# Performance work log

Hardware: AMD Instinct MI355X
Metric: run time of the kernel (lower is better)

Reference implementation:

```python
import jax, jax.numpy as jnp
import numpy as np

B, TE, TD, H, D = 8, 2048, 256, 128, 128


def setup_inputs() -> dict:
    key = jax.random.key(0)
    k1, k2, k3, k4, k5 = jax.random.split(key, 5)
    he = lambda k, shape: jax.random.normal(k, shape, dtype=jnp.float32) * jnp.sqrt(2.0 / shape[0])
    return {
        "encoder_out_seq": jax.random.normal(k1, (B, TE, H), dtype=jnp.float32),
        "decoder_out_seq": jax.random.normal(k2, (B, TD, D), dtype=jnp.float32),
        "W_a": he(k3, (H, H)),
        "U_a": he(k4, (D, H)),
        "V_a": he(k5, (H, 1)),
    }


def reference(encoder_out_seq, decoder_out_seq, W_a, U_a, V_a):
    # Precompute encoder and decoder projections once (the TF code redundantly
    # recomputes enc@W_a every decoder step inside backend.rnn).
    Wenc = jnp.einsum('bth,hk->btk', encoder_out_seq, W_a)      # [B,Te,H]
    Udec = jnp.einsum('bjd,dk->bjk', decoder_out_seq, U_a)     # [B,Td,H]
    # Additive (Bahdanau) scores: v^T tanh(W s_i + U h_j)
    scores = jnp.einsum('bjtk,k->bjt',
                        jnp.tanh(Wenc[:, None, :, :] + Udec[:, :, None, :]),
                        V_a[:, 0])                              # [B,Td,Te]
    e_outputs = jax.nn.softmax(scores, axis=-1)                 # [B,Td,Te]
    c_outputs = jnp.einsum('bjt,bth->bjh', e_outputs, encoder_out_seq)  # [B,Td,H]
    return c_outputs, e_outputs
```

## Files before the change

kernel.cpp:

```cpp
#include <hip/hip_runtime.h>
#include <stdint.h>

#define B  8
#define TE 2048
#define TD 256
#define H  128

#define FMA4(acc, s, wv) \
  acc.x += (s)*(wv).x; acc.y += (s)*(wv).y; acc.z += (s)*(wv).z; acc.w += (s)*(wv).w

__global__ __launch_bounds__(256) void proj_kernel(
    const float* __restrict__ enc, const float* __restrict__ dec,
    const float* __restrict__ Wa,  const float* __restrict__ Ua,
    float* __restrict__ EgT, float* __restrict__ Fg) {
  __shared__ float Ls[16 * 132];
  const float C2 = 2.8853900817779268f;
  int tid = threadIdx.x;
  int bid = blockIdx.x;
  bool isE = (bid < 1024);
  int rbase = (isE ? bid : bid - 1024) * 16;
  const float* in = isE ? enc : dec;
  const float* Mg = isE ? Wa : Ua;
  int hq = tid & 31, rq = tid >> 5;
  int h0 = hq * 4, r0 = rq * 2;
  const float* rowp = in + (size_t)(rbase + r0) * H;
  const float* wp = Mg + h0;
  float4 a0{0,0,0,0}, a1{0,0,0,0};
  #pragma unroll 2
  for (int kb = 0; kb < 32; ++kb) {
    float4 rv0 = *(const float4*)(rowp + kb * 4);
    float4 rv1 = *(const float4*)(rowp + H + kb * 4);
    float4 w0 = *(const float4*)(wp + (size_t)(4 * kb + 0) * H);
    float4 w1 = *(const float4*)(wp + (size_t)(4 * kb + 1) * H);
    float4 w2 = *(const float4*)(wp + (size_t)(4 * kb + 2) * H);
    float4 w3 = *(const float4*)(wp + (size_t)(4 * kb + 3) * H);
    FMA4(a0, rv0.x, w0); FMA4(a0, rv0.y, w1); FMA4(a0, rv0.z, w2); FMA4(a0, rv0.w, w3);
    FMA4(a1, rv1.x, w0); FMA4(a1, rv1.y, w1); FMA4(a1, rv1.z, w2); FMA4(a1, rv1.w, w3);
  }
  float4 e0, e1;
  e0.x = __builtin_amdgcn_exp2f(a0.x * C2); e0.y = __builtin_amdgcn_exp2f(a0.y * C2);
  e0.z = __builtin_amdgcn_exp2f(a0.z * C2); e0.w = __builtin_amdgcn_exp2f(a0.w * C2);
  e1.x = __builtin_amdgcn_exp2f(a1.x * C2); e1.y = __builtin_amdgcn_exp2f(a1.y * C2);
  e1.z = __builtin_amdgcn_exp2f(a1.z * C2); e1.w = __builtin_amdgcn_exp2f(a1.w * C2);
  if (isE) {
    *(float4*)&Ls[(r0 + 0) * 132 + h0] = e0;
    *(float4*)&Ls[(r0 + 1) * 132 + h0] = e1;
    __syncthreads();
    int b_e = rbase >> 11, t_in = rbase & 2047;
    int tb = t_in >> 6, toff = t_in & 63;
    float* dst = EgT + ((size_t)(b_e * 32 + tb) * 128) * 64 + toff;
    #pragma unroll
    for (int jj = 0; jj < 8; ++jj) {
      int idx = jj * 256 + tid;
      int r = idx & 15, k = idx >> 4;
      dst[(size_t)k * 64 + r] = Ls[r * 132 + k];
    }
  } else {
    int b_f = rbase >> 8, j_in = rbase & 255;
    float* dst = Fg + ((size_t)(b_f * TD + j_in + r0)) * H + h0;
    *(float4*)(dst + 0 * H) = e0;
    *(float4*)(dst + 1 * H) = e1;
  }
}

__global__ __launch_bounds__(512, 4) void fused_kernel(
    const float* __restrict__ EgT, const float* __restrict__ Fg,
    const float* __restrict__ Va,  const float* __restrict__ enc,
    float* __restrict__ oute, float* __restrict__ outc) {
  __shared__ float S[4 * 2048];
  __shared__ float red[16];
  int tid = threadIdx.x;
  int bid = blockIdx.x;
  int b = bid & 7, jt = bid >> 3;
  int j0 = jt * 4;
  int lane = tid & 63, w = tid >> 6;
  const float4* vp = (const float4*)Va;
  float V1 = 0.f;
  #pragma unroll
  for (int q = 0; q < 32; ++q) { float4 v = vp[q]; V1 += v.x + v.y + v.z + v.w; }

  const float4* Fp = (const float4*)(Fg + (size_t)(b * TD + j0) * H);
  const float* Ep[4];
  #pragma unroll
  for (int it = 0; it < 4; ++it)
    Ep[it] = EgT + ((size_t)(b * 32 + w + 8 * it) * 128) * 64 + lane;
  float s[4][4];
  #pragma unroll
  for (int it = 0; it < 4; ++it)
    #pragma unroll
    for (int j = 0; j < 4; ++j) s[it][j] = 0.f;
  float eka[8], ekb[8];

#define LOADE(dst, base, off)                                        \
  { const float* _p = (base) + (off);                                \
    dst[0] = _p[0];   dst[1] = _p[64];  dst[2] = _p[128];            \
    dst[3] = _p[192]; dst[4] = _p[256]; dst[5] = _p[320];            \
    dst[6] = _p[384]; dst[7] = _p[448]; }

#define UNIT4(accres, e0_, e1_, e2_, e3_, fv, vv)                         \
  {                                                                       \
    float d0 = fmaf(e0_, fv.x, 1.0f), d1 = fmaf(e1_, fv.y, 1.0f);        \
    float d2 = fmaf(e2_, fv.z, 1.0f), d3 = fmaf(e3_, fv.w, 1.0f);        \
    float p01 = d0 * d1, p23 = d2 * d3;                                   \
    float rP = __builtin_amdgcn_rcpf(p01 * p23);                          \
    float n01 = vv.x * d1 + vv.y * d0;                                    \
    float n23 = vv.z * d3 + vv.w * d2;                                    \
    accres = fmaf(n01 * p23 + n23 * p01, rP, accres);                     \
  }

  LOADE(eka, Ep[0], 0);
  for (int kc = 0; kc < 16; ++kc) {
    float4 f0[4], f1[4];
    const float4* fpc = Fp + kc * 2;
    #pragma unroll
    for (int j = 0; j < 4; ++j) {
      f0[j] = fpc[j * 32];
      f1[j] = fpc[j * 32 + 1];
    }
    float4 v0 = vp[kc * 2], v1 = vp[kc * 2 + 1];
    #pragma unroll
    for (int it = 0; it < 4; ++it) {
      if (it < 3) { LOADE(ekb, Ep[it + 1], kc * 512); }
      else        { LOADE(ekb, Ep[0], (kc + 1) * 512); }
      #pragma unroll
      for (int j = 0; j < 4; ++j) {
        UNIT4(s[it][j], eka[0], eka[1], eka[2], eka[3], f0[j], v0);
        UNIT4(s[it][j], eka[4], eka[5], eka[6], eka[7], f1[j], v1);
      }
      #pragma unroll
      for (int q = 0; q < 8; ++q) eka[q] = ekb[q];
    }
  }
  #pragma unroll
  for (int it = 0; it < 4; ++it) {
    int t = (w + 8 * it) * 64 + lane;
    S[0 * 2048 + t] = V1 - 2.0f * s[it][0];
    S[1 * 2048 + t] = V1 - 2.0f * s[it][1];
    S[2 * 2048 + t] = V1 - 2.0f * s[it][2];
    S[3 * 2048 + t] = V1 - 2.0f * s[it][3];
  }
  __syncthreads();

  int j = w >> 1, half = w & 1;
  int tb2 = half * 1024 + lane;
  float x[16];
  #pragma unroll
  for (int q = 0; q < 16; ++q) x[q] = S[j * 2048 + tb2 + q * 64];
  float m = x[0];
  #pragma unroll
  for (int q = 1; q < 16; ++q) m = fmaxf(m, x[q]);
  #pragma unroll
  for (int off = 32; off > 0; off >>= 1) m = fmaxf(m, __shfl_xor(m, off));
  if (lane == 0) red[w] = m;
  __syncthreads();
  m = fmaxf(red[j * 2], red[j * 2 + 1]);
  const float L2E = 1.4426950408889634f;
  float sum = 0.f;
  #pragma unroll
  for (int q = 0; q < 16; ++q) {
    x[q] = __builtin_amdgcn_exp2f((x[q] - m) * L2E);
    sum += x[q];
  }
  #pragma unroll
  for (int off = 32; off > 0; off >>= 1) sum += __shfl_xor(sum, off);
  if (lane == 0) red[8 + w] = sum;
  __syncthreads();
  float inv = 1.0f / (red[8 + j * 2] + red[8 + j * 2 + 1]);
  float* orow = oute + (size_t)(b * TD + j0 + j) * TE;
  #pragma unroll
  for (int q = 0; q < 16; ++q) {
    float e = x[q] * inv;
    int t = tb2 + q * 64;
    orow[t] = e;
    S[j * 2048 + t] = e;
  }
  __syncthreads();

  int hq = tid & 31, slice = tid >> 5;
  const float* encp = enc + ((size_t)b * TE + slice * 128) * H + hq * 4;
  const float* Se = S + slice * 128;
  float4 ac0{0,0,0,0}, ac1{0,0,0,0}, ac2{0,0,0,0}, ac3{0,0,0,0};
  float4 evA0, evA1, evA2, evA3, evB0, evB1, evB2, evB3;

#define LOADENC(d0, d1, d2, d3, t0)                         \
  d0 = *(const float4*)(encp + (size_t)(t0 + 0) * H);       \
  d1 = *(const float4*)(encp + (size_t)(t0 + 1) * H);       \
  d2 = *(const float4*)(encp + (size_t)(t0 + 2) * H);       \
  d3 = *(const float4*)(encp + (size_t)(t0 + 3) * H);

#define GROUP(t0, ex, ey, ez, ew)                                            \
  {                                                                          \
    float4 E0 = *(const float4*)&Se[0 * 2048 + (t0)];                        \
    float4 E1 = *(const float4*)&Se[1 * 2048 + (t0)];                        \
    float4 E2 = *(const float4*)&Se[2 * 2048 + (t0)];                        \
    float4 E3 = *(const float4*)&Se[3 * 2048 + (t0)];                        \
    FMA4(ac0, E0.x, ex); FMA4(ac0, E0.y, ey); FMA4(ac0, E0.z, ez); FMA4(ac0, E0.w, ew); \
    FMA4(ac1, E1.x, ex); FMA4(ac1, E1.y, ey); FMA4(ac1, E1.z, ez); FMA4(ac1, E1.w, ew); \
    FMA4(ac2, E2.x, ex); FMA4(ac2, E2.y, ey); FMA4(ac2, E2.z, ez); FMA4(ac2, E2.w, ew); \
    FMA4(ac3, E3.x, ex); FMA4(ac3, E3.y, ey); FMA4(ac3, E3.z, ez); FMA4(ac3, E3.w, ew); \
  }

  LOADENC(evA0, evA1, evA2, evA3, 0);
  #pragma unroll
  for (int tb = 0; tb < 128; tb += 8) {
    LOADENC(evB0, evB1, evB2, evB3, tb + 4);
    GROUP(tb, evA0, evA1, evA2, evA3);
    if (tb < 120) { LOADENC(evA0, evA1, evA2, evA3, tb + 8); }
    GROUP(tb + 4, evB0, evB1, evB2, evB3);
  }
  __syncthreads();
  if (slice < 8) {
    float* dst = &S[slice * 512 + hq * 4];
    *(float4*)(dst + 0 * 128) = ac0; *(float4*)(dst + 1 * 128) = ac1;
    *(float4*)(dst + 2 * 128) = ac2; *(float4*)(dst + 3 * 128) = ac3;
  }
  __syncthreads();
  if (slice >= 8) {
    float* dst = &S[(slice - 8) * 512 + hq * 4];
    #define RMW(J, AC) { float4 p = *(float4*)(dst + J * 128); \
      p.x += AC.x; p.y += AC.y; p.z += AC.z; p.w += AC.w; \
      *(float4*)(dst + J * 128) = p; }
    RMW(0, ac0) RMW(1, ac1) RMW(2, ac2) RMW(3, ac3)
    #undef RMW
  }
  __syncthreads();
  float r = 0.f;
  #pragma unroll
  for (int sl = 0; sl < 8; ++sl) r += S[sl * 512 + tid];
  outc[(size_t)(b * TD + j0 + (tid >> 7)) * H + (tid & 127)] = r;
}

extern "C" void kernel_launch(void* const* d_in, const int* in_sizes, int n_in,
                              void* d_out, int out_size, void* d_ws, size_t ws_size,
                              hipStream_t stream) {
  (void)in_sizes; (void)n_in; (void)out_size; (void)ws_size;
  const float* enc = (const float*)d_in[0];
  const float* dec = (const float*)d_in[1];
  const float* Wa  = (const float*)d_in[2];
  const float* Ua  = (const float*)d_in[3];
  const float* Va  = (const float*)d_in[4];

  float* ws  = (float*)d_ws;
  float* EgT = ws;
  float* Fg  = EgT + (size_t)B * TE * H;
  float* outc = (float*)d_out;
  float* oute = outc + (size_t)B * TD * H;

  proj_kernel<<<dim3(1152), 256, 0, stream>>>(enc, dec, Wa, Ua, EgT, Fg);
  fused_kernel<<<dim3(512), 512, 0, stream>>>(EgT, Fg, Va, enc, oute, outc);
}
```

Measured before the change: 176.0 us.

## Interleave encoder-projection pairs as float2 and use pairwise reciprocal units

Changes the transposed encoder projection layout so adjacent hidden pairs are stored together, letting the fused kernel load float2 values (4 loads instead of 8 per step) and the projection kernel write float2. The score inner unit now combines two terms per reciprocal instead of four, trading more rcp instructions for fewer multiplies and less overflow risk in the product. The register double-buffering is rewritten as explicit ping-pong between two float2 arrays, which avoids the copy loop.

```diff
diff --git a/kernel.cpp b/kernel.cpp
--- a/kernel.cpp
+++ b/kernel.cpp
@@ -48,12 +48,13 @@
     __syncthreads();
     int b_e = rbase >> 11, t_in = rbase & 2047;
     int tb = t_in >> 6, toff = t_in & 63;
-    float* dst = EgT + ((size_t)(b_e * 32 + tb) * 128) * 64 + toff;
-    #pragma unroll
-    for (int jj = 0; jj < 8; ++jj) {
+    float* dst = EgT + (size_t)(b_e * 32 + tb) * 8192 + toff * 2;
+    #pragma unroll
+    for (int jj = 0; jj < 4; ++jj) {
       int idx = jj * 256 + tid;
-      int r = idx & 15, k = idx >> 4;
-      dst[(size_t)k * 64 + r] = Ls[r * 132 + k];
+      int r = idx & 15, q = idx >> 4;
+      float2 val{Ls[r * 132 + 2 * q], Ls[r * 132 + 2 * q + 1]};
+      *(float2*)(dst + (size_t)q * 128 + r * 2) = val;
     }
   } else {
     int b_f = rbase >> 8, j_in = rbase & 255;
@@ -83,32 +84,34 @@
   const float* Ep[4];
   #pragma unroll
   for (int it = 0; it < 4; ++it)
-    Ep[it] = EgT + ((size_t)(b * 32 + w + 8 * it) * 128) * 64 + lane;
+    Ep[it] = EgT + (size_t)(b * 32 + w + 8 * it) * 8192 + lane * 2;
   float s[4][4];
   #pragma unroll
   for (int it = 0; it < 4; ++it)
     #pragma unroll
     for (int j = 0; j < 4; ++j) s[it][j] = 0.f;
-  float eka[8], ekb[8];
-
-#define LOADE(dst, base, off)                                        \
+  float2 eka[4], ekb[4];
+
+#define LOADE2(dst, base, off)                                       \
   { const float* _p = (base) + (off);                                \
-    dst[0] = _p[0];   dst[1] = _p[64];  dst[2] = _p[128];            \
-    dst[3] = _p[192]; dst[4] = _p[256]; dst[5] = _p[320];            \
-    dst[6] = _p[384]; dst[7] = _p[448]; }
-
-#define UNIT4(accres, e0_, e1_, e2_, e3_, fv, vv)                         \
-  {                                                                       \
-    float d0 = fmaf(e0_, fv.x, 1.0f), d1 = fmaf(e1_, fv.y, 1.0f);        \
-    float d2 = fmaf(e2_, fv.z, 1.0f), d3 = fmaf(e3_, fv.w, 1.0f);        \
-    float p01 = d0 * d1, p23 = d2 * d3;                                   \
-    float rP = __builtin_amdgcn_rcpf(p01 * p23);                          \
-    float n01 = vv.x * d1 + vv.y * d0;                                    \
-    float n23 = vv.z * d3 + vv.w * d2;                                    \
-    accres = fmaf(n01 * p23 + n23 * p01, rP, accres);                     \
-  }
-
-  LOADE(eka, Ep[0], 0);
+    dst[0] = *(const float2*)(_p);       dst[1] = *(const float2*)(_p + 128);  \
+    dst[2] = *(const float2*)(_p + 256); dst[3] = *(const float2*)(_p + 384); }
+
+#define UNIT(acc, ekk, jj)                                                    \
+  {                                                                           \
+    float d0, d1, a = 0.f;                                                    \
+    d0 = fmaf(ekk[0].x, f0[jj].x, 1.0f); d1 = fmaf(ekk[0].y, f0[jj].y, 1.0f); \
+    a += (v0.x * d1 + v0.y * d0) * __builtin_amdgcn_rcpf(d0 * d1);            \
+    d0 = fmaf(ekk[1].x, f0[jj].z, 1.0f); d1 = fmaf(ekk[1].y, f0[jj].w, 1.0f); \
+    a += (v0.z * d1 + v0.w * d0) * __builtin_amdgcn_rcpf(d0 * d1);            \
+    d0 = fmaf(ekk[2].x, f1[jj].x, 1.0f); d1 = fmaf(ekk[2].y, f1[jj].y, 1.0f); \
+    a += (v1.x * d1 + v1.y * d0) * __builtin_amdgcn_rcpf(d0 * d1);            \
+    d0 = fmaf(ekk[3].x, f1[jj].z, 1.0f); d1 = fmaf(ekk[3].y, f1[jj].w, 1.0f); \
+    a += (v1.z * d1 + v1.w * d0) * __builtin_amdgcn_rcpf(d0 * d1);            \
+    acc += a;                                                                 \
+  }
+
+  LOADE2(eka, Ep[0], 0);
   for (int kc = 0; kc < 16; ++kc) {
     float4 f0[4], f1[4];
     const float4* fpc = Fp + kc * 2;
@@ -118,18 +121,18 @@
       f1[j] = fpc[j * 32 + 1];
     }
     float4 v0 = vp[kc * 2], v1 = vp[kc * 2 + 1];
-    #pragma unroll
-    for (int it = 0; it < 4; ++it) {
-      if (it < 3) { LOADE(ekb, Ep[it + 1], kc * 512); }
-      else        { LOADE(ekb, Ep[0], (kc + 1) * 512); }
-      #pragma unroll
-      for (int j = 0; j < 4; ++j) {
-        UNIT4(s[it][j], eka[0], eka[1], eka[2], eka[3], f0[j], v0);
-        UNIT4(s[it][j], eka[4], eka[5], eka[6], eka[7], f1[j], v1);
-      }
-      #pragma unroll
-      for (int q = 0; q < 8; ++q) eka[q] = ekb[q];
-    }
+    LOADE2(ekb, Ep[1], kc * 512);
+    #pragma unroll
+    for (int j = 0; j < 4; ++j) UNIT(s[0][j], eka, j)
+    LOADE2(eka, Ep[2], kc * 512);
+    #pragma unroll
+    for (int j = 0; j < 4; ++j) UNIT(s[1][j], ekb, j)
+    LOADE2(ekb, Ep[3], kc * 512);
+    #pragma unroll
+    for (int j = 0; j < 4; ++j) UNIT(s[2][j], eka, j)
+    LOADE2(eka, Ep[0], (kc + 1) * 512);
+    #pragma unroll
+    for (int j = 0; j < 4; ++j) UNIT(s[3][j], ekb, j)
   }
   #pragma unroll
   for (int it = 0; it < 4; ++it) {
```

After: 167.6 us. -4.8%, faster.
